# Performance work log

Hardware: AMD Instinct MI355X
Metric: run time of the kernel (lower is better)

## Reference

```python
import jax, jax.numpy as jnp
import numpy as np
import math

B, H, D = 16384, 50, 128
NU, NI, NQ = 100000, 100000, 1000


def _attn(q, k, v, wq, bq, wk, bk, wv, bv, wo, bo):
    # _AttentionLayer: linear+relu on q/k/v, scaled dot-product attention, linear+relu on output
    q = jax.nn.relu(q @ wq + bq)          # [B,Q,D]
    k = jax.nn.relu(k @ wk + bk)          # [B,K,D]
    v = jax.nn.relu(v @ wv + bv)          # [B,K,D]
    scores = jnp.einsum('bqd,bkd->bqk', q, k) / math.sqrt(D)
    y = jnp.einsum('bqk,bkd->bqd', jax.nn.softmax(scores, axis=-1), v)
    return jax.nn.relu(y @ wo + bo)


def setup_inputs() -> dict:
    key = jax.random.key(0)
    ks = jax.random.split(key, 8)
    s = 1.0 / math.sqrt(D)
    inp = {
        'uids': jax.random.randint(ks[0], (B,), 0, NU),
        'qids': jax.random.randint(ks[1], (B,), 0, NQ),
        'u_movies': jax.random.randint(ks[2], (B, H, 2), 0, NI),
        'user_table': jax.random.normal(ks[3], (NU, D), jnp.float32) * 0.02,
        'query_table': jax.random.normal(ks[4], (NQ, D), jnp.float32) * 0.02,
        'item_table': jax.random.normal(ks[5], (NI, D), jnp.float32) * 0.02,
    }
    for i, n in enumerate(['gat', 'sem']):
        for j, p in enumerate(['q', 'k', 'v', 'o']):
            kk = jax.random.fold_in(key, 100 + i * 4 + j)
            inp[f'{n}_w{p}'] = jax.random.normal(kk, (D, D), jnp.float32) * s
            inp[f'{n}_b{p}'] = jnp.zeros((D,), jnp.float32)
    return inp


def reference(uids, qids, u_movies, user_table, query_table, item_table,
              gat_wq, gat_bq, gat_wk, gat_bk, gat_wv, gat_bv, gat_wo, gat_bo,
              sem_wq, sem_bq, sem_wk, sem_bk, sem_wv, sem_bv, sem_wo, sem_bo):
    node = user_table[uids]                       # [B,D]
    ex_node = query_table[qids]                   # [B,D] (computed but unused downstream, as in source)
    nb = item_table[u_movies[:, :, 0]]            # [B,H,D]
    # GAT over neighbor movies: query = node, keys/values = neighbor item embeddings
    agg = _attn(node[:, None, :], nb, nb,
                gat_wq, gat_bq, gat_wk, gat_bk, gat_wv, gat_bv, gat_wo, gat_bo)[:, 0]  # [B,D]
    _ = node + ex_node  # query_embedding in source (dead code on semantic path)
    keys = jnp.stack([node, agg], axis=1)         # [B,2,D]
    out = _attn(node[:, None, :], keys, keys,
                sem_wq, sem_bq, sem_wk, sem_bk, sem_wv, sem_bv, sem_wo, sem_bo)[:, 0]  # [B,D]
    return out
```

## Files before the change

### kernel.cpp

```cpp
#include <hip/hip_runtime.h>
#include <math.h>

typedef __bf16 bf16_t;
typedef bf16_t bf16x8 __attribute__((ext_vector_type(8)));
typedef float  f32x4  __attribute__((ext_vector_type(4)));
typedef unsigned short u16;

#define B_SZ   16384
#define H_SZ   50
#define NI_SZ  100000
#define SCALE  0.08838834764831845f
#define FRAG_W 32768


struct WPtrs { const float* p[8]; };

__global__ void prep_frags(WPtrs wp, u16* __restrict__ dst)
{
    int tid = blockIdx.x * 256 + threadIdx.x;
    int w = tid >> 14, idx = tid & 16383;
    int k = idx >> 7, n = idx & 127;
    float v = wp.p[w][idx];
    bf16_t hi = (bf16_t)v;
    bf16_t lo = (bf16_t)(v - (float)hi);
    int kk = k >> 5, k32 = k & 31;
    int e  = ((k32 >> 4) & 1) * 4 + (k32 & 3);
    int l4 = (k32 >> 2) & 3;
    int lane = l4 * 16 + (n & 15);
    int pos = ((kk * 8 + (n >> 4)) * 64 + lane) * 8 + e;
    union { bf16_t b; u16 u; } ch, cl; ch.b = hi; cl.b = lo;
    dst[(size_t)w * FRAG_W + pos]         = ch.u;
    dst[(size_t)w * FRAG_W + 16384 + pos] = cl.u;
}

__device__ __forceinline__ void repack8(f32x4 a0, f32x4 a1, bf16x8& hi, bf16x8& lo)
{
#pragma unroll
    for (int e = 0; e < 4; ++e) {
        bf16_t h0 = (bf16_t)a0[e]; hi[e] = h0; lo[e] = (bf16_t)(a0[e] - (float)h0);
        bf16_t h1 = (bf16_t)a1[e]; hi[4 + e] = h1; lo[4 + e] = (bf16_t)(a1[e] - (float)h1);
    }
}

__device__ __forceinline__ void gemm3(const bf16x8 ahi[4], const bf16x8 alo[4],
                                      const u16* __restrict__ fh, int lane, f32x4 acc[8])
{
#pragma unroll
    for (int kk = 0; kk < 4; ++kk)
#pragma unroll
        for (int n = 0; n < 8; ++n) {
            int foff = ((kk * 8 + n) * 64 + lane) * 8;
            bf16x8 bhi = *(const bf16x8*)(fh + foff);
            bf16x8 blo = *(const bf16x8*)(fh + 16384 + foff);
            acc[n] = __builtin_amdgcn_mfma_f32_16x16x32_bf16(ahi[kk], bhi, acc[n], 0, 0, 0);
            acc[n] = __builtin_amdgcn_mfma_f32_16x16x32_bf16(alo[kk], bhi, acc[n], 0, 0, 0);
            acc[n] = __builtin_amdgcn_mfma_f32_16x16x32_bf16(ahi[kk], blo, acc[n], 0, 0, 0);
        }
}

__device__ __forceinline__ void zero8(f32x4 acc[8])
{
#pragma unroll
    for (int n = 0; n < 8; ++n) acc[n] = (f32x4){0.f, 0.f, 0.f, 0.f};
}

__device__ __forceinline__ void load_afrags(const float* __restrict__ Ar, int l4,
                                            bf16x8 ahi[4], bf16x8 alo[4])
{
#pragma unroll
    for (int kk = 0; kk < 4; ++kk) {
        f32x4 a0 = *(const f32x4*)(Ar + kk * 32 + 4 * l4);
        f32x4 a1 = *(const f32x4*)(Ar + kk * 32 + 16 + 4 * l4);
        repack8(a0, a1, ahi[kk], alo[kk]);
    }
}

__device__ __forceinline__ void store_c(float* __restrict__ dst, const f32x4 acc[8],
                                        const float* __restrict__ bias,
                                        int row0, int l15, int l4)
{
#pragma unroll
    for (int n = 0; n < 8; ++n) {
        float bv = bias[n * 16 + l15];
#pragma unroll
        for (int r = 0; r < 4; ++r) {
            float v = acc[n][r] + bv;
            v = v > 0.f ? v : 0.f;
            dst[(size_t)(row0 + l4 * 4 + r) * 128 + n * 16 + l15] = v;
        }
    }
}

__device__ __forceinline__ void lds_c_write(float* __restrict__ Sw, const float vals[8][4],
                                            int l15, int l4)
{
#pragma unroll
    for (int n = 0; n < 8; ++n)
#pragma unroll
        for (int r = 0; r < 4; ++r)
            Sw[(l4 * 4 + r) * 132 + n * 16 + l15] = vals[n][r];
}

__device__ __forceinline__ void lds_read_afrags(const float* __restrict__ Sw, int l15, int l4,
                                                bf16x8 ahi[4], bf16x8 alo[4])
{
#pragma unroll
    for (int kk = 0; kk < 4; ++kk) {
        f32x4 a0 = *(const f32x4*)(Sw + l15 * 132 + kk * 32 + 4 * l4);
        f32x4 a1 = *(const f32x4*)(Sw + l15 * 132 + kk * 32 + 16 + 4 * l4);
        repack8(a0, a1, ahi[kk], alo[kk]);
    }
}

#define LGKM_FENCE() do { \
    __asm__ volatile("s_waitcnt lgkmcnt(0)" ::: "memory"); \
    __builtin_amdgcn_sched_barrier(0); } while (0)

__global__ __launch_bounds__(256, 4)
void item_kv(const float* __restrict__ A, const u16* __restrict__ frags,
             const float* __restrict__ bk, const float* __restrict__ bv,
             u16* __restrict__ kt, u16* __restrict__ vt)
{
    __shared__ u16 bounce[4 * 16 * 136];
    const int t = threadIdx.x, wave = t >> 6, lane = t & 63;
    const int l15 = lane & 15, l4 = lane >> 4;
    const int totalUnits = (NI_SZ >> 4) * 2;

    for (int unit = blockIdx.x * 4 + wave; unit < totalUnits; unit += gridDim.x * 4) {
        const int w = unit & 1, tile = unit >> 1;
        const int row0 = tile * 16;
        const float* bias = w ? bv : bk;
        u16* out = w ? vt : kt;
        const u16* fh = frags + (size_t)(w ? 2 : 1) * FRAG_W;

        const float* Ar = A + (size_t)(row0 + l15) * 128;
        bf16x8 ahi[4];
#pragma unroll
        for (int kk = 0; kk < 4; ++kk) {
            f32x4 a0 = *(const f32x4*)(Ar + kk * 32 + 4 * l4);
            f32x4 a1 = *(const f32x4*)(Ar + kk * 32 + 16 + 4 * l4);
#pragma unroll
            for (int e = 0; e < 4; ++e) {
                ahi[kk][e]     = (bf16_t)a0[e];
                ahi[kk][4 + e] = (bf16_t)a1[e];
            }
        }

        f32x4 acc[8];
        zero8(acc);
#pragma unroll
        for (int kk = 0; kk < 4; ++kk)
#pragma unroll
            for (int n = 0; n < 8; ++n) {
                int foff = ((kk * 8 + n) * 64 + lane) * 8;
                bf16x8 bhi = *(const bf16x8*)(fh + foff);
                acc[n] = __builtin_amdgcn_mfma_f32_16x16x32_bf16(ahi[kk], bhi, acc[n], 0, 0, 0);
            }

        u16* bb = bounce + wave * (16 * 136);
#pragma unroll
        for (int n = 0; n < 8; ++n) {
            float bvn = bias[n * 16 + l15];
#pragma unroll
            for (int r = 0; r < 4; ++r) {
                float v = acc[n][r] + bvn;
                v = v > 0.f ? v : 0.f;
                union { bf16_t b; u16 u; } c; c.b = (bf16_t)v;
                bb[(l4 * 4 + r) * 136 + n * 16 + l15] = c.u;
            }
        }
        LGKM_FENCE();
#pragma unroll
        for (int j = 0; j < 4; ++j) {
            int row = j * 4 + l4;
            const u16* sp = bb + row * 136 + l15 * 8;
            u16* ob = out + (size_t)(row0 + row) * 128 + l15 * 8;
            *(ulonglong2*)ob = *(const ulonglong2*)sp;
        }
        LGKM_FENCE();
    }
}

__global__ __launch_bounds__(256, 1)
void node4_fused(const float* __restrict__ ut, const int* __restrict__ uids,
                 const u16* __restrict__ frags,
                 const float* __restrict__ gbq, const float* __restrict__ sbq,
                 const float* __restrict__ sbk, const float* __restrict__ sbv,
                 float* __restrict__ qg, float* __restrict__ qs,
                 float* __restrict__ v1, float* __restrict__ d1g)
{
    const int t = threadIdx.x, wave = t >> 6, lane = t & 63;
    const int l15 = lane & 15, l4 = lane >> 4;
    const int tile = blockIdx.x * 4 + wave;
    const int row0 = tile * 16;

    const float* Ar = ut + (size_t)uids[row0 + l15] * 128;
    bf16x8 ahi[4], alo[4];
    load_afrags(Ar, l4, ahi, alo);

    f32x4 acc[8];

    zero8(acc);
    gemm3(ahi, alo, frags + 0 * FRAG_W, lane, acc);
    store_c(qg, acc, gbq, row0, l15, l4);

    float qsr[8][4];
    zero8(acc);
    gemm3(ahi, alo, frags + 4 * FRAG_W, lane, acc);
#pragma unroll
    for (int n = 0; n < 8; ++n) {
        float bv = sbq[n * 16 + l15];
#pragma unroll
        for (int r = 0; r < 4; ++r) {
            float v = acc[n][r] + bv;
            qsr[n][r] = v > 0.f ? v : 0.f;
            qs[(size_t)(row0 + l4 * 4 + r) * 128 + n * 16 + l15] = qsr[n][r];
        }
    }

    zero8(acc);
    gemm3(ahi, alo, frags + 5 * FRAG_W, lane, acc);
    float d1[4] = {0.f, 0.f, 0.f, 0.f};
#pragma unroll
    for (int n = 0; n < 8; ++n) {
        float bv = sbk[n * 16 + l15];
#pragma unroll
        for (int r = 0; r < 4; ++r) {
            float v = acc[n][r] + bv;
            v = v > 0.f ? v : 0.f;
            d1[r] += qsr[n][r] * v;
        }
    }
#pragma unroll
    for (int r = 0; r < 4; ++r) {
#pragma unroll
        for (int off = 8; off; off >>= 1) d1[r] += __shfl_xor(d1[r], off);
    }
    if (l15 == 0) {
#pragma unroll
        for (int r = 0; r < 4; ++r) d1g[row0 + l4 * 4 + r] = d1[r];
    }

    zero8(acc);
    gemm3(ahi, alo, frags + 6 * FRAG_W, lane, acc);
    store_c(v1, acc, sbv, row0, l15, l4);
}

__global__ __launch_bounds__(256)
void gat_attn(const float* __restrict__ qg, const u16* __restrict__ kt,
              const u16* __restrict__ vt, const int* __restrict__ um,
              float* __restrict__ y)
{
    __shared__ float qsh[4][128];
    const int wave = threadIdx.x >> 6, lane = threadIdx.x & 63;
    const int b = blockIdx.x * 4 + wave;

    float2 q2 = *(const float2*)(qg + (size_t)b * 128 + lane * 2);
    qsh[wave][lane * 2]     = q2.x;
    qsh[wave][lane * 2 + 1] = q2.y;

    int mrow = (lane < H_SZ) ? um[((size_t)b * H_SZ + lane) * 2] : 0;

    unsigned vreg[H_SZ];
#pragma unroll
    for (int h = 0; h < H_SZ; ++h) {
        int vr = __shfl(mrow, h);
        vreg[h] = *(const unsigned*)(vt + (size_t)vr * 128 + lane * 2);
    }
    __syncthreads();

    float s = -1e30f;
    if (lane < H_SZ) {
        const u16* kr = kt + (size_t)mrow * 128;
        float acc = 0.f;
#pragma unroll
        for (int c = 0; c < 4; ++c) {
            bf16x8 kc[4];
#pragma unroll
            for (int j = 0; j < 4; ++j) kc[j] = *(const bf16x8*)(kr + (c * 4 + j) * 8);
#pragma unroll
            for (int j = 0; j < 4; ++j)
#pragma unroll
                for (int e = 0; e < 8; ++e)
                    acc += (float)kc[j][e] * qsh[wave][(c * 4 + j) * 8 + e];
        }
        s = acc * SCALE;
    }
    float m = s;
#pragma unroll
    for (int off = 32; off; off >>= 1) m = fmaxf(m, __shfl_xor(m, off));
    float p = (lane < H_SZ) ? __expf(s - m) : 0.f;
    float sum = p;
#pragma unroll
    for (int off = 32; off; off >>= 1) sum += __shfl_xor(sum, off);
    p /= sum;

    float ax = 0.f, ay = 0.f;
#pragma unroll
    for (int h = 0; h < H_SZ; ++h) {
        float ph = __shfl(p, h);
        unsigned u = vreg[h];
        ax += ph * __uint_as_float(u << 16);
        ay += ph * __uint_as_float(u & 0xffff0000u);
    }
    *(float2*)(y + (size_t)b * 128 + lane * 2) = (float2){ax, ay};
}

__global__ __launch_bounds__(256, 1)
void sem_fused(const float* __restrict__ yb, const float* __restrict__ qs,
               const float* __restrict__ v1, const float* __restrict__ d1g,
               const u16* __restrict__ frags,
               const float* __restrict__ gbo, const float* __restrict__ sbk,
               const float* __restrict__ sbv, const float* __restrict__ sbo,
               float* __restrict__ outf)
{
    __shared__ float S[4][16 * 132];
    const int t = threadIdx.x, wave = t >> 6, lane = t & 63;
    const int l15 = lane & 15, l4 = lane >> 4;
    float* Sw = S[wave];
    const int tile = blockIdx.x * 4 + wave;
    const int row0 = tile * 16;

    bf16x8 ahi[4], alo[4];
    load_afrags(yb + (size_t)(row0 + l15) * 128, l4, ahi, alo);
    f32x4 acc[8];
    zero8(acc);
    gemm3(ahi, alo, frags + 3 * FRAG_W, lane, acc);

    float stg[8][4];
#pragma unroll
    for (int n = 0; n < 8; ++n) {
        float bv = gbo[n * 16 + l15];
#pragma unroll
        for (int r = 0; r < 4; ++r) {
            float v = acc[n][r] + bv;
            stg[n][r] = v > 0.f ? v : 0.f;
        }
    }
    lds_c_write(Sw, stg, l15, l4);
    LGKM_FENCE();
    lds_read_afrags(Sw, l15, l4, ahi, alo);

    float k2r[8][4], v2r[8][4];
    zero8(acc);
    gemm3(ahi, alo, frags + 5 * FRAG_W, lane, acc);
#pragma unroll
    for (int n = 0; n < 8; ++n) {
        float bv = sbk[n * 16 + l15];
#pragma unroll
        for (int r = 0; r < 4; ++r) {
            float v = acc[n][r] + bv;
            k2r[n][r] = v > 0.f ? v : 0.f;
        }
    }
    zero8(acc);
    gemm3(ahi, alo, frags + 6 * FRAG_W, lane, acc);
#pragma unroll
    for (int n = 0; n < 8; ++n) {
        float bv = sbv[n * 16 + l15];
#pragma unroll
        for (int r = 0; r < 4; ++r) {
            float v = acc[n][r] + bv;
            v2r[n][r] = v > 0.f ? v : 0.f;
        }
    }

    float d2[4] = {0.f, 0.f, 0.f, 0.f};
#pragma unroll
    for (int n = 0; n < 8; ++n) {
#pragma unroll
        for (int r = 0; r < 4; ++r) {
            float q = qs[(size_t)(row0 + l4 * 4 + r) * 128 + n * 16 + l15];
            d2[r] += q * k2r[n][r];
        }
    }
#pragma unroll
    for (int r = 0; r < 4; ++r) {
#pragma unroll
        for (int off = 8; off; off >>= 1) d2[r] += __shfl_xor(d2[r], off);
    }
    float p1[4], p2[4];
#pragma unroll
    for (int r = 0; r < 4; ++r) {
        float s1 = d1g[row0 + l4 * 4 + r] * SCALE;
        float s2 = d2[r] * SCALE;
        float m = fmaxf(s1, s2);
        float e1 = __expf(s1 - m), e2 = __expf(s2 - m);
        float inv = 1.f / (e1 + e2);
        p1[r] = e1 * inv; p2[r] = e2 * inv;
    }
#pragma unroll
    for (int n = 0; n < 8; ++n) {
#pragma unroll
        for (int r = 0; r < 4; ++r) {
            float vv1 = v1[(size_t)(row0 + l4 * 4 + r) * 128 + n * 16 + l15];
            stg[n][r] = p1[r] * vv1 + p2[r] * v2r[n][r];
        }
    }

    LGKM_FENCE();
    lds_c_write(Sw, stg, l15, l4);
    LGKM_FENCE();
    lds_read_afrags(Sw, l15, l4, ahi, alo);
    zero8(acc);
    gemm3(ahi, alo, frags + 7 * FRAG_W, lane, acc);
    store_c(outf, acc, sbo, row0, l15, l4);
}

extern "C" void kernel_launch(void* const* d_in, const int* in_sizes, int n_in,
                              void* d_out, int out_size, void* d_ws, size_t ws_size,
                              hipStream_t stream)
{
    const int*   uids       = (const int*)d_in[0];
    const int*   um         = (const int*)d_in[2];
    const float* user_table = (const float*)d_in[3];
    const float* item_table = (const float*)d_in[5];
    const float* gwq = (const float*)d_in[6];  const float* gbq = (const float*)d_in[7];
    const float* gwk = (const float*)d_in[8];  const float* gbk = (const float*)d_in[9];
    const float* gwv = (const float*)d_in[10]; const float* gbv = (const float*)d_in[11];
    const float* gwo = (const float*)d_in[12]; const float* gbo = (const float*)d_in[13];
    const float* swq = (const float*)d_in[14]; const float* sbq = (const float*)d_in[15];
    const float* swk = (const float*)d_in[16]; const float* sbk = (const float*)d_in[17];
    const float* swv = (const float*)d_in[18]; const float* sbv = (const float*)d_in[19];
    const float* swo = (const float*)d_in[20]; const float* sbo = (const float*)d_in[21];

    char* ws = (char*)d_ws;
    u16*   kt    = (u16*)ws;   ws += (size_t)NI_SZ * 128 * 2;
    u16*   vt    = (u16*)ws;   ws += (size_t)NI_SZ * 128 * 2;
    u16*   frags = (u16*)ws;   ws += (size_t)8 * FRAG_W * 2;
    float* qg  = (float*)ws;   ws += (size_t)B_SZ * 128 * 4;
    float* qs  = (float*)ws;   ws += (size_t)B_SZ * 128 * 4;
    float* v1  = (float*)ws;   ws += (size_t)B_SZ * 128 * 4;
    float* yb  = (float*)ws;   ws += (size_t)B_SZ * 128 * 4;
    float* d1g = (float*)ws;   ws += (size_t)B_SZ * 4;
    float* outf = (float*)d_out;

    WPtrs wp; wp.p[0]=gwq; wp.p[1]=gwk; wp.p[2]=gwv; wp.p[3]=gwo;
              wp.p[4]=swq; wp.p[5]=swk; wp.p[6]=swv; wp.p[7]=swo;
    prep_frags<<<512, 256, 0, stream>>>(wp, frags);

    item_kv<<<3125, 256, 0, stream>>>(item_table, frags, gbk, gbv, kt, vt);

    node4_fused<<<256, 256, 0, stream>>>(user_table, uids, frags,
                                         gbq, sbq, sbk, sbv, qg, qs, v1, d1g);

    gat_attn<<<B_SZ / 4, 256, 0, stream>>>(qg, kt, vt, um, yb);

    sem_fused<<<256, 256, 0, stream>>>(yb, qs, v1, d1g, frags,
                                       gbo, sbk, sbv, sbo, outf);
}
```

Measured before the change: 326.7 us.

## Split node/sem GEMM columns across waves and stage item_kv weights in LDS

```diff
diff --git a/kernel.cpp b/kernel.cpp
--- a/kernel.cpp
+++ b/kernel.cpp
@@ -42,26 +42,22 @@
     }
 }
 
-__device__ __forceinline__ void gemm3(const bf16x8 ahi[4], const bf16x8 alo[4],
-                                      const u16* __restrict__ fh, int lane, f32x4 acc[8])
+template<int NB>
+__device__ __forceinline__ void gemm3_nb(const bf16x8 ahi[4], const bf16x8 alo[4],
+                                         const u16* __restrict__ fh, int lane, int n0,
+                                         f32x4 acc[NB])
 {
 #pragma unroll
     for (int kk = 0; kk < 4; ++kk)
 #pragma unroll
-        for (int n = 0; n < 8; ++n) {
-            int foff = ((kk * 8 + n) * 64 + lane) * 8;
+        for (int ni = 0; ni < NB; ++ni) {
+            int foff = ((kk * 8 + (n0 + ni)) * 64 + lane) * 8;
             bf16x8 bhi = *(const bf16x8*)(fh + foff);
             bf16x8 blo = *(const bf16x8*)(fh + 16384 + foff);
-            acc[n] = __builtin_amdgcn_mfma_f32_16x16x32_bf16(ahi[kk], bhi, acc[n], 0, 0, 0);
-            acc[n] = __builtin_amdgcn_mfma_f32_16x16x32_bf16(alo[kk], bhi, acc[n], 0, 0, 0);
-            acc[n] = __builtin_amdgcn_mfma_f32_16x16x32_bf16(ahi[kk], blo, acc[n], 0, 0, 0);
-        }
-}
-
-__device__ __forceinline__ void zero8(f32x4 acc[8])
-{
-#pragma unroll
-    for (int n = 0; n < 8; ++n) acc[n] = (f32x4){0.f, 0.f, 0.f, 0.f};
+            acc[ni] = __builtin_amdgcn_mfma_f32_16x16x32_bf16(ahi[kk], bhi, acc[ni], 0, 0, 0);
+            acc[ni] = __builtin_amdgcn_mfma_f32_16x16x32_bf16(alo[kk], bhi, acc[ni], 0, 0, 0);
+            acc[ni] = __builtin_amdgcn_mfma_f32_16x16x32_bf16(ahi[kk], blo, acc[ni], 0, 0, 0);
+        }
 }
 
 __device__ __forceinline__ void load_afrags(const float* __restrict__ Ar, int l4,
@@ -75,39 +71,13 @@
     }
 }
 
-__device__ __forceinline__ void store_c(float* __restrict__ dst, const f32x4 acc[8],
-                                        const float* __restrict__ bias,
-                                        int row0, int l15, int l4)
-{
-#pragma unroll
-    for (int n = 0; n < 8; ++n) {
-        float bv = bias[n * 16 + l15];
-#pragma unroll
-        for (int r = 0; r < 4; ++r) {
-            float v = acc[n][r] + bv;
-            v = v > 0.f ? v : 0.f;
-            dst[(size_t)(row0 + l4 * 4 + r) * 128 + n * 16 + l15] = v;
-        }
-    }
-}
-
-__device__ __forceinline__ void lds_c_write(float* __restrict__ Sw, const float vals[8][4],
-                                            int l15, int l4)
-{
-#pragma unroll
-    for (int n = 0; n < 8; ++n)
-#pragma unroll
-        for (int r = 0; r < 4; ++r)
-            Sw[(l4 * 4 + r) * 132 + n * 16 + l15] = vals[n][r];
-}
-
-__device__ __forceinline__ void lds_read_afrags(const float* __restrict__ Sw, int l15, int l4,
+__device__ __forceinline__ void lds_read_afrags(const float* __restrict__ S, int l15, int l4,
                                                 bf16x8 ahi[4], bf16x8 alo[4])
 {
 #pragma unroll
     for (int kk = 0; kk < 4; ++kk) {
-        f32x4 a0 = *(const f32x4*)(Sw + l15 * 132 + kk * 32 + 4 * l4);
-        f32x4 a1 = *(const f32x4*)(Sw + l15 * 132 + kk * 32 + 16 + 4 * l4);
+        f32x4 a0 = *(const f32x4*)(S + l15 * 132 + kk * 32 + 4 * l4);
+        f32x4 a1 = *(const f32x4*)(S + l15 * 132 + kk * 32 + 16 + 4 * l4);
         repack8(a0, a1, ahi[kk], alo[kk]);
     }
 }
@@ -121,17 +91,30 @@
              const float* __restrict__ bk, const float* __restrict__ bv,
              u16* __restrict__ kt, u16* __restrict__ vt)
 {
+    __shared__ u16 Bh[16384];
     __shared__ u16 bounce[4 * 16 * 136];
     const int t = threadIdx.x, wave = t >> 6, lane = t & 63;
     const int l15 = lane & 15, l4 = lane >> 4;
-    const int totalUnits = (NI_SZ >> 4) * 2;
-
-    for (int unit = blockIdx.x * 4 + wave; unit < totalUnits; unit += gridDim.x * 4) {
-        const int w = unit & 1, tile = unit >> 1;
+    const int w = blockIdx.x & 1;
+    const int blkw = blockIdx.x >> 1;
+    const float* bias = w ? bv : bk;
+    u16* out = w ? vt : kt;
+    const u16* fh = frags + (size_t)(w ? 2 : 1) * FRAG_W;
+
+#pragma unroll
+    for (int j = 0; j < 8; ++j)
+        *(ulonglong2*)(Bh + t * 64 + j * 8) = *(const ulonglong2*)(fh + t * 64 + j * 8);
+    __syncthreads();
+
+    float bvn[8];
+#pragma unroll
+    for (int n = 0; n < 8; ++n) bvn[n] = bias[n * 16 + l15];
+
+    const int NT = NI_SZ >> 4;
+    for (int tb = blkw * 4; tb < NT; tb += 512 * 4) {
+        const int tile = tb + wave;
+        if (tile >= NT) break;
         const int row0 = tile * 16;
-        const float* bias = w ? bv : bk;
-        u16* out = w ? vt : kt;
-        const u16* fh = frags + (size_t)(w ? 2 : 1) * FRAG_W;
 
         const float* Ar = A + (size_t)(row0 + l15) * 128;
         bf16x8 ahi[4];
@@ -147,28 +130,26 @@
         }
 
         f32x4 acc[8];
-        zero8(acc);
+#pragma unroll
+        for (int n = 0; n < 8; ++n) acc[n] = (f32x4){0.f, 0.f, 0.f, 0.f};
 #pragma unroll
         for (int kk = 0; kk < 4; ++kk)
 #pragma unroll
             for (int n = 0; n < 8; ++n) {
-                int foff = ((kk * 8 + n) * 64 + lane) * 8;
-                bf16x8 bhi = *(const bf16x8*)(fh + foff);
+                bf16x8 bhi = *(const bf16x8*)(Bh + ((kk * 8 + n) * 64 + lane) * 8);
                 acc[n] = __builtin_amdgcn_mfma_f32_16x16x32_bf16(ahi[kk], bhi, acc[n], 0, 0, 0);
             }
 
         u16* bb = bounce + wave * (16 * 136);
 #pragma unroll
-        for (int n = 0; n < 8; ++n) {
-            float bvn = bias[n * 16 + l15];
+        for (int n = 0; n < 8; ++n)
 #pragma unroll
             for (int r = 0; r < 4; ++r) {
-                float v = acc[n][r] + bvn;
+                float v = acc[n][r] + bvn[n];
                 v = v > 0.f ? v : 0.f;
                 union { bf16_t b; u16 u; } c; c.b = (bf16_t)v;
                 bb[(l4 * 4 + r) * 136 + n * 16 + l15] = c.u;
             }
-        }
         LGKM_FENCE();
 #pragma unroll
         for (int j = 0; j < 4; ++j) {
@@ -181,7 +162,7 @@
     }
 }
 
-__global__ __launch_bounds__(256, 1)
+__global__ __launch_bounds__(256, 4)
 void node4_fused(const float* __restrict__ ut, const int* __restrict__ uids,
                  const u16* __restrict__ frags,
                  const float* __restrict__ gbq, const float* __restrict__ sbq,
@@ -189,46 +170,55 @@
                  float* __restrict__ qg, float* __restrict__ qs,
                  float* __restrict__ v1, float* __restrict__ d1g)
 {
+    __shared__ float dpart[4][16];
     const int t = threadIdx.x, wave = t >> 6, lane = t & 63;
     const int l15 = lane & 15, l4 = lane >> 4;
-    const int tile = blockIdx.x * 4 + wave;
-    const int row0 = tile * 16;
+    const int n0 = wave * 2;
+    const int row0 = blockIdx.x * 16;
 
     const float* Ar = ut + (size_t)uids[row0 + l15] * 128;
     bf16x8 ahi[4], alo[4];
     load_afrags(Ar, l4, ahi, alo);
 
-    f32x4 acc[8];
-
-    zero8(acc);
-    gemm3(ahi, alo, frags + 0 * FRAG_W, lane, acc);
-    store_c(qg, acc, gbq, row0, l15, l4);
-
-    float qsr[8][4];
-    zero8(acc);
-    gemm3(ahi, alo, frags + 4 * FRAG_W, lane, acc);
-#pragma unroll
-    for (int n = 0; n < 8; ++n) {
-        float bv = sbq[n * 16 + l15];
-#pragma unroll
-        for (int r = 0; r < 4; ++r) {
-            float v = acc[n][r] + bv;
-            qsr[n][r] = v > 0.f ? v : 0.f;
-            qs[(size_t)(row0 + l4 * 4 + r) * 128 + n * 16 + l15] = qsr[n][r];
-        }
-    }
-
-    zero8(acc);
-    gemm3(ahi, alo, frags + 5 * FRAG_W, lane, acc);
+    f32x4 acc[2];
+
+    acc[0] = (f32x4){0,0,0,0}; acc[1] = (f32x4){0,0,0,0};
+    gemm3_nb<2>(ahi, alo, frags + 0 * FRAG_W, lane, n0, acc);
+#pragma unroll
+    for (int ni = 0; ni < 2; ++ni) {
+        float bv = gbq[(n0 + ni) * 16 + l15];
+#pragma unroll
+        for (int r = 0; r < 4; ++r) {
+            float v = acc[ni][r] + bv;
+            qg[(size_t)(row0 + l4 * 4 + r) * 128 + (n0 + ni) * 16 + l15] = v > 0.f ? v : 0.f;
+        }
+    }
+
+    float qsr[2][4];
+    acc[0] = (f32x4){0,0,0,0}; acc[1] = (f32x4){0,0,0,0};
+    gemm3_nb<2>(ahi, alo, frags + 4 * FRAG_W, lane, n0, acc);
+#pragma unroll
+    for (int ni = 0; ni < 2; ++ni) {
+        float bv = sbq[(n0 + ni) * 16 + l15];
+#pragma unroll
+        for (int r = 0; r < 4; ++r) {
+            float v = acc[ni][r] + bv;
+            qsr[ni][r] = v > 0.f ? v : 0.f;
+            qs[(size_t)(row0 + l4 * 4 + r) * 128 + (n0 + ni) * 16 + l15] = qsr[ni][r];
+        }
+    }
+
+    acc[0] = (f32x4){0,0,0,0}; acc[1] = (f32x4){0,0,0,0};
+    gemm3_nb<2>(ahi, alo, frags + 5 * FRAG_W, lane, n0, acc);
     float d1[4] = {0.f, 0.f, 0.f, 0.f};
 #pragma unroll
-    for (int n = 0; n < 8; ++n) {
-        float bv = sbk[n * 16 + l15];
-#pragma unroll
-        for (int r = 0; r < 4; ++r) {
-            float v = acc[n][r] + bv;
+    for (int ni = 0; ni < 2; ++ni) {
+        float bv = sbk[(n0 + ni) * 16 + l15];
+#pragma unroll
+        for (int r = 0; r < 4; ++r) {
+            float v = acc[ni][r] + bv;
             v = v > 0.f ? v : 0.f;
-            d1[r] += qsr[n][r] * v;
+            d1[r] += qsr[ni][r] * v;
         }
     }
 #pragma unroll
@@ -238,12 +228,24 @@
     }
     if (l15 == 0) {
 #pragma unroll
-        for (int r = 0; r < 4; ++r) d1g[row0 + l4 * 4 + r] = d1[r];
-    }
-
-    zero8(acc);
-    gemm3(ahi, alo, frags + 6 * FRAG_W, lane, acc);
-    store_c(v1, acc, sbv, row0, l15, l4);
+        for (int r = 0; r < 4; ++r) dpart[wave][l4 * 4 + r] = d1[r];
+    }
+
+    acc[0] = (f32x4){0,0,0,0}; acc[1] = (f32x4){0,0,0,0};
+    gemm3_nb<2>(ahi, alo, frags + 6 * FRAG_W, lane, n0, acc);
+#pragma unroll
+    for (int ni = 0; ni < 2; ++ni) {
+        float bv = sbv[(n0 + ni) * 16 + l15];
+#pragma unroll
+        for (int r = 0; r < 4; ++r) {
+            float v = acc[ni][r] + bv;
+            v1[(size_t)(row0 + l4 * 4 + r) * 128 + (n0 + ni) * 16 + l15] = v > 0.f ? v : 0.f;
+        }
+    }
+
+    __syncthreads();
+    if (t < 16)
+        d1g[row0 + t] = dpart[0][t] + dpart[1][t] + dpart[2][t] + dpart[3][t];
 }
 
 __global__ __launch_bounds__(256)
@@ -306,7 +308,7 @@
     *(float2*)(y + (size_t)b * 128 + lane * 2) = (float2){ax, ay};
 }
 
-__global__ __launch_bounds__(256, 1)
+__global__ __launch_bounds__(256, 4)
 void sem_fused(const float* __restrict__ yb, const float* __restrict__ qs,
                const float* __restrict__ v1, const float* __restrict__ d1g,
                const u16* __restrict__ frags,
@@ -314,97 +316,108 @@
                const float* __restrict__ sbv, const float* __restrict__ sbo,
                float* __restrict__ outf)
 {
-    __shared__ float S[4][16 * 132];
+    __shared__ float S[16 * 132];
+    __shared__ float dpart[4][16];
     const int t = threadIdx.x, wave = t >> 6, lane = t & 63;
     const int l15 = lane & 15, l4 = lane >> 4;
-    float* Sw = S[wave];
-    const int tile = blockIdx.x * 4 + wave;
-    const int row0 = tile * 16;
+    const int n0 = wave * 2;
+    const int row0 = blockIdx.x * 16;
 
     bf16x8 ahi[4], alo[4];
     load_afrags(yb + (size_t)(row0 + l15) * 128, l4, ahi, alo);
-    f32x4 acc[8];
-    zero8(acc);
-    gemm3(ahi, alo, frags + 3 * FRAG_W, lane, acc);
-
-    float stg[8][4];
-#pragma unroll
-    for (int n = 0; n < 8; ++n) {
-        float bv = gbo[n * 16 + l15];
-#pragma unroll
-        for (int r = 0; r < 4; ++r) {
-            float v = acc[n][r] + bv;
-            stg[n][r] = v > 0.f ? v : 0.f;
-        }
-    }
-    lds_c_write(Sw, stg, l15, l4);
-    LGKM_FENCE();
-    lds_read_afrags(Sw, l15, l4, ahi, alo);
-
-    float k2r[8][4], v2r[8][4];
-    zero8(acc);
-    gemm3(ahi, alo, frags + 5 * FRAG_W, lane, acc);
-#pragma unroll
-    for (int n = 0; n < 8; ++n) {
-        float bv = sbk[n * 16 + l15];
-#pragma unroll
-        for (int r = 0; r < 4; ++r) {
-            float v = acc[n][r] + bv;
-            k2r[n][r] = v > 0.f ? v : 0.f;
-        }
-    }
-    zero8(acc);
-    gemm3(ahi, alo, frags + 6 * FRAG_W, lane, acc);
-#pragma unroll
-    for (int n = 0; n < 8; ++n) {
-        float bv = sbv[n * 16 + l15];
-#pragma unroll
-        for (int r = 0; r < 4; ++r) {
-            float v = acc[n][r] + bv;
-            v2r[n][r] = v > 0.f ? v : 0.f;
+    f32x4 acc[2];
+    acc[0] = (f32x4){0,0,0,0}; acc[1] = (f32x4){0,0,0,0};
+    gemm3_nb<2>(ahi, alo, frags + 3 * FRAG_W, lane, n0, acc);
+#pragma unroll
+    for (int ni = 0; ni < 2; ++ni) {
+        float bv = gbo[(n0 + ni) * 16 + l15];
+#pragma unroll
+        for (int r = 0; r < 4; ++r) {
+            float v = acc[ni][r] + bv;
+            S[(l4 * 4 + r) * 132 + (n0 + ni) * 16 + l15] = v > 0.f ? v : 0.f;
+        }
+    }
+    __syncthreads();
+    lds_read_afrags(S, l15, l4, ahi, alo);
+
+    float k2c[2][4], v2c[2][4];
+    acc[0] = (f32x4){0,0,0,0}; acc[1] = (f32x4){0,0,0,0};
+    gemm3_nb<2>(ahi, alo, frags + 5 * FRAG_W, lane, n0, acc);
+#pragma unroll
+    for (int ni = 0; ni < 2; ++ni) {
+        float bv = sbk[(n0 + ni) * 16 + l15];
+#pragma unroll
+        for (int r = 0; r < 4; ++r) {
+            float v = acc[ni][r] + bv;
+            k2c[ni][r] = v > 0.f ? v : 0.f;
+        }
+    }
+    acc[0] = (f32x4){0,0,0,0}; acc[1] = (f32x4){0,0,0,0};
+    gemm3_nb<2>(ahi, alo, frags + 6 * FRAG_W, lane, n0, acc);
+#pragma unroll
+    for (int ni = 0; ni < 2; ++ni) {
+        float bv = sbv[(n0 + ni) * 16 + l15];
+#pragma unroll
+        for (int r = 0; r < 4; ++r) {
+            float v = acc[ni][r] + bv;
+            v2c[ni][r] = v > 0.f ? v : 0.f;
         }
     }
 
     float d2[4] = {0.f, 0.f, 0.f, 0.f};
-#pragma unroll
-    for (int n = 0; n < 8; ++n) {
-#pragma unroll
-        for (int r = 0; r < 4; ++r) {
-            float q = qs[(size_t)(row0 + l4 * 4 + r) * 128 + n * 16 + l15];
-            d2[r] += q * k2r[n][r];
-        }
-    }
+    float qsv[2][4];
+#pragma unroll
+    for (int ni = 0; ni < 2; ++ni)
+#pragma unroll
+        for (int r = 0; r < 4; ++r) {
+            qsv[ni][r] = qs[(size_t)(row0 + l4 * 4 + r) * 128 + (n0 + ni) * 16 + l15];
+            d2[r] += qsv[ni][r] * k2c[ni][r];
+        }
+    (void)qsv;
 #pragma unroll
     for (int r = 0; r < 4; ++r) {
 #pragma unroll
         for (int off = 8; off; off >>= 1) d2[r] += __shfl_xor(d2[r], off);
     }
+    if (l15 == 0) {
+#pragma unroll
+        for (int r = 0; r < 4; ++r) dpart[wave][l4 * 4 + r] = d2[r];
+    }
+    __syncthreads();
+
     float p1[4], p2[4];
 #pragma unroll
     for (int r = 0; r < 4; ++r) {
-        float s1 = d1g[row0 + l4 * 4 + r] * SCALE;
-        float s2 = d2[r] * SCALE;
+        int ridx = l4 * 4 + r;
+        float d2t = dpart[0][ridx] + dpart[1][ridx] + dpart[2][ridx] + dpart[3][ridx];
+        float s1 = d1g[row0 + ridx] * SCALE;
+        float s2 = d2t * SCALE;
         float m = fmaxf(s1, s2);
         float e1 = __expf(s1 - m), e2 = __expf(s2 - m);
         float inv = 1.f / (e1 + e2);
         p1[r] = e1 * inv; p2[r] = e2 * inv;
     }
 #pragma unroll
-    for (int n = 0; n < 8; ++n) {
-#pragma unroll
-        for (int r = 0; r < 4; ++r) {
-            float vv1 = v1[(size_t)(row0 + l4 * 4 + r) * 128 + n * 16 + l15];
-            stg[n][r] = p1[r] * vv1 + p2[r] * v2r[n][r];
-        }
-    }
-
-    LGKM_FENCE();
-    lds_c_write(Sw, stg, l15, l4);
-    LGKM_FENCE();
-    lds_read_afrags(Sw, l15, l4, ahi, alo);
-    zero8(acc);
-    gemm3(ahi, alo, frags + 7 * FRAG_W, lane, acc);
-    store_c(outf, acc, sbo, row0, l15, l4);
+    for (int ni = 0; ni < 2; ++ni)
+#pragma unroll
+        for (int r = 0; r < 4; ++r) {
+            float vv1 = v1[(size_t)(row0 + l4 * 4 + r) * 128 + (n0 + ni) * 16 + l15];
+            S[(l4 * 4 + r) * 132 + (n0 + ni) * 16 + l15] = p1[r] * vv1 + p2[r] * v2c[ni][r];
+        }
+    __syncthreads();
+    lds_read_afrags(S, l15, l4, ahi, alo);
+
+    acc[0] = (f32x4){0,0,0,0}; acc[1] = (f32x4){0,0,0,0};
+    gemm3_nb<2>(ahi, alo, frags + 7 * FRAG_W, lane, n0, acc);
+#pragma unroll
+    for (int ni = 0; ni < 2; ++ni) {
+        float bv = sbo[(n0 + ni) * 16 + l15];
+#pragma unroll
+        for (int r = 0; r < 4; ++r) {
+            float v = acc[ni][r] + bv;
+            outf[(size_t)(row0 + l4 * 4 + r) * 128 + (n0 + ni) * 16 + l15] = v > 0.f ? v : 0.f;
+        }
+    }
 }
 
 extern "C" void kernel_launch(void* const* d_in, const int* in_sizes, int n_in,
@@ -439,13 +452,13 @@
               wp.p[4]=swq; wp.p[5]=swk; wp.p[6]=swv; wp.p[7]=swo;
     prep_frags<<<512, 256, 0, stream>>>(wp, frags);
 
-    item_kv<<<3125, 256, 0, stream>>>(item_table, frags, gbk, gbv, kt, vt);
-
-    node4_fused<<<256, 256, 0, stream>>>(user_table, uids, frags,
-                                         gbq, sbq, sbk, sbv, qg, qs, v1, d1g);
+    item_kv<<<1024, 256, 0, stream>>>(item_table, frags, gbk, gbv, kt, vt);
+
+    node4_fused<<<1024, 256, 0, stream>>>(user_table, uids, frags,
+                                          gbq, sbq, sbk, sbv, qg, qs, v1, d1g);
 
     gat_attn<<<B_SZ / 4, 256, 0, stream>>>(qg, kt, vt, um, yb);
 
-    sem_fused<<<256, 256, 0, stream>>>(yb, qs, v1, d1g, frags,
-                                       gbo, sbk, sbv, sbo, outf);
-}
+    sem_fused<<<1024, 256, 0, stream>>>(yb, qs, v1, d1g, frags,
+                                        gbo, sbk, sbv, sbo, outf);
+}
```

Result: faster. 276.5 us (-15.4%).
